# Kernel optimization log

Measured on AMD Instinct MI355X. Metric: run time of the kernel, lower is better.

The kernel has to match this reference:

```python
import jax, jax.numpy as jnp
import numpy as np

B, S, P, I = 32, 64, 32, 256
NF, H, L = 4, 512, 2
OUT = 2
INITRANGE = 0.1
assert NF * I == 2 * H  # layer-2 GRU input dim equals layer-1 input dim


def setup_inputs() -> dict:
    key = jax.random.key(0)
    ks = jax.random.split(key, 12)
    u = lambda k, shape: jax.random.uniform(k, shape, jnp.float32, -INITRANGE, INITRANGE)
    return {
        "inputs": jax.random.normal(ks[0], (B, S, P, I), jnp.float32),
        "inputs_demoip": jax.random.normal(ks[1], (B, 3), jnp.float32),
        "conv_w": u(ks[2], (NF, I)),            # Conv1d(1, NF, kernel=I) == dot product
        "conv_b": u(ks[3], (NF,)),
        "conv2_w": u(ks[4], (2 * H,)),          # Conv1d(1, 1, kernel=2H) == dot product
        "conv2_b": u(ks[5], (1,)),
        "wih": u(ks[6], (L, 2, 3 * H, NF * I)),  # [layer, dir, 3H, in]
        "whh": u(ks[7], (L, 2, 3 * H, H)),
        "bih": u(ks[8], (L, 2, 3 * H)),
        "bhh": u(ks[9], (L, 2, 3 * H)),
        "lin_w": u(ks[10], (OUT, 2 * H + 3)),
        "lin_b": u(ks[11], (OUT,)),
        "batch_size": B,
    }


def _gru_dir(x, wih, whh, bih, bhh, reverse):
    """One direction of a torch-style GRU. x: [B,S,in] -> [B,S,H]."""
    gx = jnp.einsum('bsi,gi->bsg', x, wih) + bih  # precompute input gates [B,S,3H]
    if reverse:
        gx = gx[:, ::-1]
    h0 = jnp.zeros((x.shape[0], H), x.dtype)

    def step(h, gxt):
        gh = h @ whh.T + bhh
        xr, xz, xn = jnp.split(gxt, 3, axis=-1)
        hr, hz, hn = jnp.split(gh, 3, axis=-1)
        r = jax.nn.sigmoid(xr + hr)
        z = jax.nn.sigmoid(xz + hz)
        n = jnp.tanh(xn + r * hn)
        h_new = (1.0 - z) * n + z * h
        return h_new, h_new

    _, ys = jax.lax.scan(step, h0, gx.transpose(1, 0, 2))
    ys = ys.transpose(1, 0, 2)  # [B,S,H]
    if reverse:
        ys = ys[:, ::-1]
    return ys


def reference(inputs, inputs_demoip, conv_w, conv_b, conv2_w, conv2_b,
              wih, whh, bih, bhh, lin_w, lin_b, batch_size):
    # --- convolutional attention embedding (kernel spans full input -> dot product) ---
    scores = jnp.einsum('bspi,fi->bsfp', inputs, conv_w) + conv_b[None, None, :, None]
    conv_wts = jax.nn.softmax(scores, axis=-1)                    # softmax over pad dim
    vec = jnp.einsum('bsfp,bspi->bsfi', conv_wts, inputs)         # [B,S,NF,I]
    embedding = vec.reshape(batch_size, S, NF * I)                # [B,S,NF*I]

    # --- stacked bidirectional GRU (eval mode: dropout omitted) ---
    x = embedding
    for l in range(L):
        f = _gru_dir(x, wih[l, 0], whh[l, 0], bih[l, 0], bhh[l, 0], False)
        b = _gru_dir(x, wih[l, 1], whh[l, 1], bih[l, 1], bhh[l, 1], True)
        x = jnp.concatenate([f, b], axis=-1)
    states = x                                                    # [B,S,2H]

    # --- second attention (conv2 kernel spans 2H -> dot product per step) ---
    alpha = jax.nn.softmax(states @ conv2_w + conv2_b[0], axis=1)  # [B,S]
    context = jnp.einsum('bs,bsh->bh', alpha, states)              # [B,2H]

    context_v2 = jnp.concatenate([context, inputs_demoip], axis=1)  # [B,2H+3]
    out = jax.nn.softmax(context_v2 @ lin_w.T + lin_b, axis=1)      # [B,OUT]
    return out, conv_wts, states, context, alpha
```

## Files before the change

### kernel.cpp

```cpp
#include <hip/hip_runtime.h>

typedef __attribute__((ext_vector_type(8))) short s8v;
typedef __attribute__((ext_vector_type(8))) __bf16 bf8v;
typedef __attribute__((ext_vector_type(4))) float f32x4;
typedef unsigned long long ULL;

#define DEVINL __device__ __forceinline__

DEVINL unsigned short f2bf(float f) {
    unsigned int x = __float_as_uint(f);
    unsigned int r = (x + 0x7FFFu + ((x >> 16) & 1u)) >> 16;
    return (unsigned short)r;
}

DEVINL f32x4 mfma16(s8v a, s8v b, f32x4 c) {
    return __builtin_amdgcn_mfma_f32_16x16x32_bf16(
        __builtin_bit_cast(bf8v, a), __builtin_bit_cast(bf8v, b), c, 0, 0, 0);
}

typedef const __attribute__((address_space(1))) unsigned int gu32;
typedef __attribute__((address_space(3))) unsigned int lu32;
DEVINL void gload16(const void* g, unsigned int lds_off) {
    __builtin_amdgcn_global_load_lds((gu32*)g, (lu32*)(size_t)lds_off, 16, 0, 0);
}

#define WS_CTR   0
#define WS_HBUF  4096
#define WS_ZERO_BYTES 266240
#define WS_WIH   266240
#define WS_WHH   (WS_WIH + 12582912)
#define WS_EMB   (WS_WHH + 6291456)
#define WS_ST1   (WS_EMB + 4194304)
#define WS_GX    (WS_ST1 + 4194304)

__global__ __launch_bounds__(256) void k_cvt(const float* __restrict__ in,
                                             unsigned short* __restrict__ out, int n) {
    int i0 = (blockIdx.x * 256 + threadIdx.x) * 8;
    if (i0 + 8 > n) return;
    f32x4 a = *(const f32x4*)(in + i0);
    f32x4 b = *(const f32x4*)(in + i0 + 4);
    s8v o;
    o[0] = (short)f2bf(a[0]); o[1] = (short)f2bf(a[1]);
    o[2] = (short)f2bf(a[2]); o[3] = (short)f2bf(a[3]);
    o[4] = (short)f2bf(b[0]); o[5] = (short)f2bf(b[1]);
    o[6] = (short)f2bf(b[2]); o[7] = (short)f2bf(b[3]);
    *(s8v*)(out + i0) = o;
}

__global__ __launch_bounds__(256) void k_conv(const float* __restrict__ inp,
                                              const float* __restrict__ conv_w,
                                              const float* __restrict__ conv_b,
                                              float* __restrict__ wts_out,
                                              unsigned short* __restrict__ emb) {
    const int bs = blockIdx.x, tid = threadIdx.x;
    __shared__ float xs[32][260];
    __shared__ float sc[4][32];
    __shared__ float wts[4][32];
    const float* x = inp + (size_t)bs * 8192;
    {
        int p = tid >> 3, i0 = (tid & 7) * 32;
        const float* src = x + p * 256 + i0;
        float* dst = &xs[p][i0];
#pragma unroll
        for (int j = 0; j < 32; j += 4) *(f32x4*)(dst + j) = *(const f32x4*)(src + j);
    }
    __syncthreads();
    {
        int p = tid >> 3, o = tid & 7;
        float s0 = 0, s1 = 0, s2 = 0, s3 = 0;
        const float* xp = &xs[p][o * 32];
#pragma unroll
        for (int j = 0; j < 32; j += 4) {
            f32x4 v  = *(const f32x4*)(xp + j);
            f32x4 w0 = *(const f32x4*)(conv_w + o * 32 + j);
            f32x4 w1 = *(const f32x4*)(conv_w + 256 + o * 32 + j);
            f32x4 w2 = *(const f32x4*)(conv_w + 512 + o * 32 + j);
            f32x4 w3 = *(const f32x4*)(conv_w + 768 + o * 32 + j);
#pragma unroll
            for (int q = 0; q < 4; ++q) {
                s0 += v[q] * w0[q]; s1 += v[q] * w1[q];
                s2 += v[q] * w2[q]; s3 += v[q] * w3[q];
            }
        }
#pragma unroll
        for (int d = 4; d; d >>= 1) {
            s0 += __shfl_down(s0, d, 8); s1 += __shfl_down(s1, d, 8);
            s2 += __shfl_down(s2, d, 8); s3 += __shfl_down(s3, d, 8);
        }
        if (o == 0) {
            sc[0][p] = s0 + conv_b[0]; sc[1][p] = s1 + conv_b[1];
            sc[2][p] = s2 + conv_b[2]; sc[3][p] = s3 + conv_b[3];
        }
    }
    __syncthreads();
    if (tid < 4) {
        float mx = -1e30f;
        for (int p = 0; p < 32; ++p) mx = fmaxf(mx, sc[tid][p]);
        float sm = 0.f;
        for (int p = 0; p < 32; ++p) { float e = __expf(sc[tid][p] - mx); wts[tid][p] = e; sm += e; }
        float inv = 1.f / sm;
        for (int p = 0; p < 32; ++p) wts[tid][p] *= inv;
    }
    __syncthreads();
    if (tid < 128) wts_out[(size_t)bs * 128 + tid] = wts[tid >> 5][tid & 31];
    {
        float a0 = 0, a1 = 0, a2 = 0, a3 = 0;
#pragma unroll 8
        for (int p = 0; p < 32; ++p) {
            float v = xs[p][tid];
            a0 += wts[0][p] * v; a1 += wts[1][p] * v;
            a2 += wts[2][p] * v; a3 += wts[3][p] * v;
        }
        unsigned short* e = emb + (size_t)bs * 1024;
        e[tid] = f2bf(a0); e[256 + tid] = f2bf(a1);
        e[512 + tid] = f2bf(a2); e[768 + tid] = f2bf(a3);
    }
}

__global__ __launch_bounds__(256, 2) void k_gemm(const unsigned short* __restrict__ A,
                                                 const unsigned short* __restrict__ B,
                                                 const float* __restrict__ bias,
                                                 const float* __restrict__ bias2,
                                                 float* __restrict__ C,
                                                 int M, int N, int K) {
    const int bm = blockIdx.y * 128, bn = blockIdx.x * 128;
    const int tid = threadIdx.x, w = tid >> 6, l = tid & 63;
    const int wr = w >> 1, wc = w & 1;
    const int lr = l & 15, lq = l >> 4;

    __shared__ __align__(1024) unsigned short As[8192];
    __shared__ __align__(1024) unsigned short Bs[8192];
    const unsigned int AsOff = (unsigned int)(size_t)(void*)As;
    const unsigned int BsOff = (unsigned int)(size_t)(void*)Bs;

    f32x4 acc[4][4] = {};
    const int srow = tid >> 3;
    const int scol = ((tid & 7) ^ (srow & 7)) * 8;
    const unsigned int ldsW = w * 1024 + (l << 4);

    for (int k0 = 0; k0 < K; k0 += 64) {
        __syncthreads();
#pragma unroll
        for (int j = 0; j < 4; ++j)
            gload16(A + (size_t)(bm + j * 32 + srow) * K + k0 + scol,
                    AsOff + j * 4096 + (ldsW - (l << 4)));
#pragma unroll
        for (int j = 0; j < 4; ++j)
            gload16(B + (size_t)(bn + j * 32 + srow) * K + k0 + scol,
                    BsOff + j * 4096 + (ldsW - (l << 4)));
        asm volatile("s_waitcnt vmcnt(0)" ::: "memory");
        __syncthreads();
#pragma unroll
        for (int kk = 0; kk < 2; ++kk) {
            s8v af[4], bf_[4];
#pragma unroll
            for (int mt = 0; mt < 4; ++mt) {
                const int row = wr * 64 + mt * 16 + lr;
                const int qg = kk * 4 + lq;
                af[mt] = *(const s8v*)((const char*)As + row * 128 +
                                       ((qg ^ (row & 7)) << 4));
            }
#pragma unroll
            for (int nt = 0; nt < 4; ++nt) {
                const int row = wc * 64 + nt * 16 + lr;
                const int qg = kk * 4 + lq;
                bf_[nt] = *(const s8v*)((const char*)Bs + row * 128 +
                                        ((qg ^ (row & 7)) << 4));
            }
#pragma unroll
            for (int mt = 0; mt < 4; ++mt)
#pragma unroll
                for (int nt = 0; nt < 4; ++nt)
                    acc[mt][nt] = mfma16(af[mt], bf_[nt], acc[mt][nt]);
        }
    }
#pragma unroll
    for (int mt = 0; mt < 4; ++mt)
#pragma unroll
        for (int nt = 0; nt < 4; ++nt)
#pragma unroll
            for (int r = 0; r < 4; ++r) {
                int row = bm + wr * 64 + mt * 16 + lq * 4 + r;
                int col = bn + wc * 64 + nt * 16 + lr;
                int gg = col >> 9;
                float b2 = (gg != 2 && gg != 5) ? bias2[col] : 0.f;
                C[(size_t)row * N + col] = acc[mt][nt][r] + bias[col] + b2;
            }
}

__global__ __launch_bounds__(256, 1) void k_scan(const float* __restrict__ gx,
                                                 const unsigned short* __restrict__ whh,
                                                 const float* __restrict__ bhh,
                                                 unsigned short* __restrict__ hbuf,
                                                 unsigned int* __restrict__ flags,
                                                 float* __restrict__ st32,
                                                 unsigned short* __restrict__ st16) {
    const int blk = blockIdx.x;
    const int dir = blk >> 3, jg = blk & 7;
    const int tid = threadIdx.x;
    const int w = tid >> 6, l = tid & 63;
    const int lr = l & 15, lq = l >> 4;
    const int jb = jg * 64;
    const int mycol = jb + w * 16 + lr;

    __shared__ __align__(1024) unsigned short hs[16384];

    s8v bf[3][16];
#pragma unroll
    for (int g = 0; g < 3; ++g) {
        const unsigned short* wr =
            whh + ((size_t)dir * 1536 + g * 512 + mycol) * 512 + lq * 8;
#pragma unroll
        for (int kt = 0; kt < 16; ++kt) bf[g][kt] = *(const s8v*)(wr + kt * 32);
    }
    const float bh_n = bhh[dir * 1536 + 1024 + mycol];

    unsigned short* hb0 = hbuf + (size_t)dir * 32768;
    unsigned int* fl = flags + dir * 128;
    unsigned int* myflag = fl + jg * 16;

    float hp[2][4] = {{0.f, 0.f, 0.f, 0.f}, {0.f, 0.f, 0.f, 0.f}};

    for (int t = 0; t < 64; ++t) {
        const int s = dir ? (63 - t) : t;
        float pg[3][2][4];
#pragma unroll
        for (int g = 0; g < 3; ++g)
#pragma unroll
            for (int bt = 0; bt < 2; ++bt)
#pragma unroll
                for (int r = 0; r < 4; ++r) {
                    const int b = bt * 16 + lq * 4 + r;
                    pg[g][bt][r] = gx[(size_t)(b * 64 + s) * 3072 + dir * 1536 +
                                      g * 512 + mycol];
                }
        if (t > 0) {
            if (w == 0 && l < 8) {
                while (__hip_atomic_load(&fl[l * 16], __ATOMIC_RELAXED,
                                         __HIP_MEMORY_SCOPE_AGENT) < (unsigned)t)
                    __builtin_amdgcn_s_sleep(1);
            }
            __syncthreads();
        }
        const unsigned short* hc = hb0 + (size_t)(t & 1) * 16384;
#pragma unroll
        for (int i = 0; i < 8; ++i) {
            const int c = tid + 256 * i;
            const int row = c >> 6, inb = (c & 63) * 16;
            const ULL* hq = (const ULL*)(hc + c * 8);
            ULL d0 = __hip_atomic_load(hq, __ATOMIC_RELAXED, __HIP_MEMORY_SCOPE_AGENT);
            ULL d1 = __hip_atomic_load(hq + 1, __ATOMIC_RELAXED, __HIP_MEMORY_SCOPE_AGENT);
            char* dst = (char*)hs + row * 1024 + (inb ^ ((row & 7) << 4));
            *(ULL*)dst = d0;
            *(ULL*)(dst + 8) = d1;
        }
        __syncthreads();
        f32x4 acc[3][2] = {};
#pragma unroll
        for (int bt = 0; bt < 2; ++bt) {
            const int row = bt * 16 + lr;
            const int m = (row & 7) << 4;
#pragma unroll
            for (int kt = 0; kt < 16; ++kt) {
                s8v a = *(const s8v*)((const char*)hs + row * 1024 +
                                      ((kt * 64 + lq * 16) ^ m));
                acc[0][bt] = mfma16(a, bf[0][kt], acc[0][bt]);
                acc[1][bt] = mfma16(a, bf[1][kt], acc[1][bt]);
                acc[2][bt] = mfma16(a, bf[2][kt], acc[2][bt]);
            }
        }
        unsigned short* hnw = hb0 + (size_t)((t + 1) & 1) * 16384;
        float hnew[2][4];
#pragma unroll
        for (int bt = 0; bt < 2; ++bt)
#pragma unroll
            for (int r = 0; r < 4; ++r) {
                const int b = bt * 16 + lq * 4 + r;
                float r_ = __builtin_amdgcn_rcpf(
                    1.f + __expf(-(pg[0][bt][r] + acc[0][bt][r])));
                float z_ = __builtin_amdgcn_rcpf(
                    1.f + __expf(-(pg[1][bt][r] + acc[1][bt][r])));
                float q = pg[2][bt][r] + r_ * (acc[2][bt][r] + bh_n);
                q = fminf(fmaxf(q, -15.f), 15.f);
                float e = __expf(2.f * q);
                float n_ = (e - 1.f) * __builtin_amdgcn_rcpf(e + 1.f);
                float h = (1.f - z_) * n_ + z_ * hp[bt][r];
                hp[bt][r] = h;
                hnew[bt][r] = h;
                __hip_atomic_store(&hnw[b * 512 + mycol], f2bf(h), __ATOMIC_RELAXED,
                                   __HIP_MEMORY_SCOPE_AGENT);
            }
        __syncthreads();
        if (tid == 0 && t < 63)
            __hip_atomic_store(myflag, (unsigned)(t + 1), __ATOMIC_RELAXED,
                               __HIP_MEMORY_SCOPE_AGENT);
#pragma unroll
        for (int bt = 0; bt < 2; ++bt)
#pragma unroll
            for (int r = 0; r < 4; ++r) {
                const int b = bt * 16 + lq * 4 + r;
                const size_t so = (size_t)(b * 64 + s) * 1024 + dir * 512 + mycol;
                if (st32) st32[so] = hnew[bt][r];
                if (st16) st16[so] = f2bf(hnew[bt][r]);
            }
    }
}

__global__ __launch_bounds__(256) void k_finale(const float* __restrict__ states,
                                                const float* __restrict__ conv2_w,
                                                const float* __restrict__ conv2_b,
                                                const float* __restrict__ demoip,
                                                const float* __restrict__ lin_w,
                                                const float* __restrict__ lin_b,
                                                float* __restrict__ out,
                                                float* __restrict__ context,
                                                float* __restrict__ alpha) {
    const int b = blockIdx.x, tid = threadIdx.x, w = tid >> 6, l = tid & 63;
    __shared__ float dots[64], al[64], ctx[1024], lg[2];
    const float* st = states + (size_t)b * 65536;
    for (int si = 0; si < 16; ++si) {
        int s = w * 16 + si;
        const float* row = st + s * 1024;
        float sum = 0.f;
        for (int i = l; i < 1024; i += 64) sum += row[i] * conv2_w[i];
#pragma unroll
        for (int m = 32; m; m >>= 1) sum += __shfl_xor(sum, m, 64);
        if (l == 0) dots[s] = sum + conv2_b[0];
    }
    __syncthreads();
    if (w == 0) {
        float v = dots[l];
        float mx = v;
#pragma unroll
        for (int m = 32; m; m >>= 1) mx = fmaxf(mx, __shfl_xor(mx, m, 64));
        float e = __expf(v - mx);
        float sm = e;
#pragma unroll
        for (int m = 32; m; m >>= 1) sm += __shfl_xor(sm, m, 64);
        float a = e / sm;
        al[l] = a;
        alpha[b * 64 + l] = a;
    }
    __syncthreads();
    for (int h = tid; h < 1024; h += 256) {
        float c = 0.f;
#pragma unroll 8
        for (int s = 0; s < 64; ++s) c += al[s] * st[s * 1024 + h];
        ctx[h] = c;
        context[b * 1024 + h] = c;
    }
    __syncthreads();
    if (w < 2) {
        const float* lw = lin_w + w * 1027;
        float sum = 0.f;
        for (int i = l; i < 1024; i += 64) sum += ctx[i] * lw[i];
#pragma unroll
        for (int m = 32; m; m >>= 1) sum += __shfl_xor(sum, m, 64);
        if (l == 0) {
            sum += lw[1024] * demoip[b * 3] + lw[1025] * demoip[b * 3 + 1] +
                   lw[1026] * demoip[b * 3 + 2] + lin_b[w];
            lg[w] = sum;
        }
    }
    __syncthreads();
    if (tid == 0) {
        float m = fmaxf(lg[0], lg[1]);
        float e0 = __expf(lg[0] - m), e1 = __expf(lg[1] - m);
        float inv = 1.f / (e0 + e1);
        out[b * 2 + 0] = e0 * inv;
        out[b * 2 + 1] = e1 * inv;
    }
}

extern "C" void kernel_launch(void* const* d_in, const int* in_sizes, int n_in,
                              void* d_out, int out_size, void* d_ws, size_t ws_size,
                              hipStream_t stream) {
    const float* inputs  = (const float*)d_in[0];
    const float* demoip  = (const float*)d_in[1];
    const float* conv_w  = (const float*)d_in[2];
    const float* conv_b  = (const float*)d_in[3];
    const float* conv2_w = (const float*)d_in[4];
    const float* conv2_b = (const float*)d_in[5];
    const float* wih     = (const float*)d_in[6];
    const float* whh     = (const float*)d_in[7];
    const float* bih     = (const float*)d_in[8];
    const float* bhh     = (const float*)d_in[9];
    const float* lin_w   = (const float*)d_in[10];
    const float* lin_b   = (const float*)d_in[11];

    char* ws = (char*)d_ws;
    unsigned int* ctrs    = (unsigned int*)(ws + WS_CTR);
    unsigned short* hbuf  = (unsigned short*)(ws + WS_HBUF);
    unsigned short* wih16 = (unsigned short*)(ws + WS_WIH);
    unsigned short* whh16 = (unsigned short*)(ws + WS_WHH);
    unsigned short* emb16 = (unsigned short*)(ws + WS_EMB);
    unsigned short* st116 = (unsigned short*)(ws + WS_ST1);
    float* gxbuf          = (float*)(ws + WS_GX);

    float* out_out    = (float*)d_out;
    float* wts_out    = out_out + 64;
    float* states_out = out_out + 262208;
    float* ctx_out    = out_out + 2359360;
    float* alpha_out  = out_out + 2392128;

    hipMemsetAsync(ws, 0, WS_ZERO_BYTES, stream);
    k_cvt<<<3072, 256, 0, stream>>>(wih, wih16, 6291456);
    k_cvt<<<1536, 256, 0, stream>>>(whh, whh16, 3145728);
    k_conv<<<2048, 256, 0, stream>>>(inputs, conv_w, conv_b, wts_out, emb16);
    k_gemm<<<dim3(24, 16), 256, 0, stream>>>(emb16, wih16, bih, bhh, gxbuf,
                                             2048, 3072, 1024);
    k_scan<<<16, 256, 0, stream>>>(gxbuf, whh16, bhh, hbuf, ctrs, nullptr, st116);
    k_gemm<<<dim3(24, 16), 256, 0, stream>>>(st116, wih16 + 3145728, bih + 3072,
                                             bhh + 3072, gxbuf, 2048, 3072, 1024);
    k_scan<<<16, 256, 0, stream>>>(gxbuf, whh16 + 1572864, bhh + 3072, hbuf + 65536,
                                   ctrs + 256, states_out, nullptr);
    k_finale<<<32, 256, 0, stream>>>(states_out, conv2_w, conv2_b, demoip, lin_w, lin_b,
                                     out_out, ctx_out, alpha_out);
}
```

Before: 841.6 us.

## Use per-wave flags in GRU scan and fuse prep kernels into one launch

```diff
diff --git a/kernel.cpp b/kernel.cpp
--- a/kernel.cpp
+++ b/kernel.cpp
@@ -25,34 +25,44 @@
 }
 
 #define WS_CTR   0
-#define WS_HBUF  4096
-#define WS_ZERO_BYTES 266240
-#define WS_WIH   266240
+#define WS_HBUF  8192
+#define WS_WIH   270336
 #define WS_WHH   (WS_WIH + 12582912)
 #define WS_EMB   (WS_WHH + 6291456)
 #define WS_ST1   (WS_EMB + 4194304)
 #define WS_GX    (WS_ST1 + 4194304)
 
-__global__ __launch_bounds__(256) void k_cvt(const float* __restrict__ in,
-                                             unsigned short* __restrict__ out, int n) {
-    int i0 = (blockIdx.x * 256 + threadIdx.x) * 8;
-    if (i0 + 8 > n) return;
-    f32x4 a = *(const f32x4*)(in + i0);
-    f32x4 b = *(const f32x4*)(in + i0 + 4);
-    s8v o;
-    o[0] = (short)f2bf(a[0]); o[1] = (short)f2bf(a[1]);
-    o[2] = (short)f2bf(a[2]); o[3] = (short)f2bf(a[3]);
-    o[4] = (short)f2bf(b[0]); o[5] = (short)f2bf(b[1]);
-    o[6] = (short)f2bf(b[2]); o[7] = (short)f2bf(b[3]);
-    *(s8v*)(out + i0) = o;
-}
-
-__global__ __launch_bounds__(256) void k_conv(const float* __restrict__ inp,
+__global__ __launch_bounds__(256) void k_prep(const float* __restrict__ inp,
                                               const float* __restrict__ conv_w,
                                               const float* __restrict__ conv_b,
                                               float* __restrict__ wts_out,
-                                              unsigned short* __restrict__ emb) {
-    const int bs = blockIdx.x, tid = threadIdx.x;
+                                              unsigned short* __restrict__ emb,
+                                              const float* __restrict__ wih,
+                                              unsigned short* __restrict__ wih16,
+                                              const float* __restrict__ whh,
+                                              unsigned short* __restrict__ whh16,
+                                              unsigned int* __restrict__ flagz) {
+    const int bid = blockIdx.x, tid = threadIdx.x;
+    if (bid >= 2048) {
+        const float* src;
+        unsigned short* dst;
+        int i0;
+        if (bid < 5120) { src = wih; dst = wih16; i0 = ((bid - 2048) * 256 + tid) * 8; }
+        else            { src = whh; dst = whh16; i0 = ((bid - 5120) * 256 + tid) * 8; }
+        f32x4 a = *(const f32x4*)(src + i0);
+        f32x4 b = *(const f32x4*)(src + i0 + 4);
+        s8v o;
+        o[0] = (short)f2bf(a[0]); o[1] = (short)f2bf(a[1]);
+        o[2] = (short)f2bf(a[2]); o[3] = (short)f2bf(a[3]);
+        o[4] = (short)f2bf(b[0]); o[5] = (short)f2bf(b[1]);
+        o[6] = (short)f2bf(b[2]); o[7] = (short)f2bf(b[3]);
+        *(s8v*)(dst + i0) = o;
+        return;
+    }
+    const int bs = bid;
+    if (bs == 0) {
+        for (int i = tid; i < 2048; i += 256) flagz[i] = 0;
+    }
     __shared__ float xs[32][260];
     __shared__ float sc[4][32];
     __shared__ float wts[4][32];
@@ -203,7 +213,7 @@
     const int jb = jg * 64;
     const int mycol = jb + w * 16 + lr;
 
-    __shared__ __align__(1024) unsigned short hs[16384];
+    __shared__ __align__(1024) unsigned short hs[32768];
 
     s8v bf[3][16];
 #pragma unroll
@@ -216,8 +226,8 @@
     const float bh_n = bhh[dir * 1536 + 1024 + mycol];
 
     unsigned short* hb0 = hbuf + (size_t)dir * 32768;
-    unsigned int* fl = flags + dir * 128;
-    unsigned int* myflag = fl + jg * 16;
+    unsigned int* fl = flags + dir * 512;
+    unsigned int* myflag = fl + (jg * 4 + w) * 16;
 
     float hp[2][4] = {{0.f, 0.f, 0.f, 0.f}, {0.f, 0.f, 0.f, 0.f}};
 
@@ -234,39 +244,41 @@
                     pg[g][bt][r] = gx[(size_t)(b * 64 + s) * 3072 + dir * 1536 +
                                       g * 512 + mycol];
                 }
+        f32x4 acc[3][2] = {};
         if (t > 0) {
-            if (w == 0 && l < 8) {
-                while (__hip_atomic_load(&fl[l * 16], __ATOMIC_RELAXED,
-                                         __HIP_MEMORY_SCOPE_AGENT) < (unsigned)t)
-                    __builtin_amdgcn_s_sleep(1);
+            for (;;) {
+                bool ok = (l >= 32) ||
+                          (__hip_atomic_load(&fl[l * 16], __ATOMIC_RELAXED,
+                                             __HIP_MEMORY_SCOPE_AGENT) >= (unsigned)t);
+                if (__all(ok)) break;
+                __builtin_amdgcn_s_sleep(1);
+            }
+            const unsigned short* hc = hb0 + (size_t)(t & 1) * 16384;
+            char* hsb = (char*)hs + (t & 1) * 32768;
+#pragma unroll
+            for (int i = 0; i < 8; ++i) {
+                const int c = tid + 256 * i;
+                const int row = c >> 6, inb = (c & 63) * 16;
+                const ULL* hq = (const ULL*)(hc + c * 8);
+                ULL d0 = __hip_atomic_load(hq, __ATOMIC_RELAXED, __HIP_MEMORY_SCOPE_AGENT);
+                ULL d1 = __hip_atomic_load(hq + 1, __ATOMIC_RELAXED, __HIP_MEMORY_SCOPE_AGENT);
+                char* dst = hsb + row * 1024 + (inb ^ ((row & 7) << 4));
+                *(ULL*)dst = d0;
+                *(ULL*)(dst + 8) = d1;
             }
             __syncthreads();
-        }
-        const unsigned short* hc = hb0 + (size_t)(t & 1) * 16384;
-#pragma unroll
-        for (int i = 0; i < 8; ++i) {
-            const int c = tid + 256 * i;
-            const int row = c >> 6, inb = (c & 63) * 16;
-            const ULL* hq = (const ULL*)(hc + c * 8);
-            ULL d0 = __hip_atomic_load(hq, __ATOMIC_RELAXED, __HIP_MEMORY_SCOPE_AGENT);
-            ULL d1 = __hip_atomic_load(hq + 1, __ATOMIC_RELAXED, __HIP_MEMORY_SCOPE_AGENT);
-            char* dst = (char*)hs + row * 1024 + (inb ^ ((row & 7) << 4));
-            *(ULL*)dst = d0;
-            *(ULL*)(dst + 8) = d1;
-        }
-        __syncthreads();
-        f32x4 acc[3][2] = {};
-#pragma unroll
-        for (int bt = 0; bt < 2; ++bt) {
-            const int row = bt * 16 + lr;
-            const int m = (row & 7) << 4;
-#pragma unroll
-            for (int kt = 0; kt < 16; ++kt) {
-                s8v a = *(const s8v*)((const char*)hs + row * 1024 +
-                                      ((kt * 64 + lq * 16) ^ m));
-                acc[0][bt] = mfma16(a, bf[0][kt], acc[0][bt]);
-                acc[1][bt] = mfma16(a, bf[1][kt], acc[1][bt]);
-                acc[2][bt] = mfma16(a, bf[2][kt], acc[2][bt]);
+#pragma unroll
+            for (int bt = 0; bt < 2; ++bt) {
+                const int row = bt * 16 + lr;
+                const int m = (row & 7) << 4;
+#pragma unroll
+                for (int kt = 0; kt < 16; ++kt) {
+                    s8v a = *(const s8v*)((const char*)hsb + row * 1024 +
+                                          ((kt * 64 + lq * 16) ^ m));
+                    acc[0][bt] = mfma16(a, bf[0][kt], acc[0][bt]);
+                    acc[1][bt] = mfma16(a, bf[1][kt], acc[1][bt]);
+                    acc[2][bt] = mfma16(a, bf[2][kt], acc[2][bt]);
+                }
             }
         }
         unsigned short* hnw = hb0 + (size_t)((t + 1) & 1) * 16384;
@@ -290,8 +302,8 @@
                 __hip_atomic_store(&hnw[b * 512 + mycol], f2bf(h), __ATOMIC_RELAXED,
                                    __HIP_MEMORY_SCOPE_AGENT);
             }
-        __syncthreads();
-        if (tid == 0 && t < 63)
+        asm volatile("s_waitcnt vmcnt(0)" ::: "memory");
+        if (l == 0 && t < 63)
             __hip_atomic_store(myflag, (unsigned)(t + 1), __ATOMIC_RELAXED,
                                __HIP_MEMORY_SCOPE_AGENT);
 #pragma unroll
@@ -403,17 +415,15 @@
     float* ctx_out    = out_out + 2359360;
     float* alpha_out  = out_out + 2392128;
 
-    hipMemsetAsync(ws, 0, WS_ZERO_BYTES, stream);
-    k_cvt<<<3072, 256, 0, stream>>>(wih, wih16, 6291456);
-    k_cvt<<<1536, 256, 0, stream>>>(whh, whh16, 3145728);
-    k_conv<<<2048, 256, 0, stream>>>(inputs, conv_w, conv_b, wts_out, emb16);
+    k_prep<<<6656, 256, 0, stream>>>(inputs, conv_w, conv_b, wts_out, emb16,
+                                     wih, wih16, whh, whh16, ctrs);
     k_gemm<<<dim3(24, 16), 256, 0, stream>>>(emb16, wih16, bih, bhh, gxbuf,
                                              2048, 3072, 1024);
     k_scan<<<16, 256, 0, stream>>>(gxbuf, whh16, bhh, hbuf, ctrs, nullptr, st116);
     k_gemm<<<dim3(24, 16), 256, 0, stream>>>(st116, wih16 + 3145728, bih + 3072,
                                              bhh + 3072, gxbuf, 2048, 3072, 1024);
     k_scan<<<16, 256, 0, stream>>>(gxbuf, whh16 + 1572864, bhh + 3072, hbuf + 65536,
-                                   ctrs + 256, states_out, nullptr);
+                                   ctrs + 1024, states_out, nullptr);
     k_finale<<<32, 256, 0, stream>>>(states_out, conv2_w, conv2_b, demoip, lin_w, lin_b,
                                      out_out, ctx_out, alpha_out);
 }
```

Result: slower. 879.5 us (+4.5%).
